# Optimization experiments

Hardware: AMD Instinct MI355X
Metric: run time of the kernel (lower is better)

## Reference

```python
import jax, jax.numpy as jnp
import numpy as np

DIM = 128
NUM_HEADS = 4
HEAD_DIM = DIM // NUM_HEADS
WINDOW = 7
N = WINDOW * WINDOW
B = 16384
SCALE = HEAD_DIM ** -0.5


def _relative_position_index(window_size: int) -> np.ndarray:
    coords_h = np.arange(window_size)
    coords_w = np.arange(window_size)
    coords = np.stack(np.meshgrid(coords_h, coords_w, indexing='ij'))  # [2, w, w]
    coords_flatten = coords.reshape(2, -1)  # [2, w*w]
    rel = coords_flatten[:, :, None] - coords_flatten[:, None, :]  # [2, N, N]
    rel = rel.transpose(1, 2, 0).copy()
    rel[:, :, 0] += window_size - 1
    rel[:, :, 1] += window_size - 1
    rel[:, :, 0] *= 2 * window_size - 1
    return rel.sum(-1).astype(np.int32)  # [N, N]


def setup_inputs() -> dict:
    key = jax.random.key(0)
    ks = jax.random.split(key, 8)
    x = jax.random.normal(ks[0], (B, N, DIM), dtype=jnp.float32)
    q_global = jax.random.normal(ks[1], (B, 1, DIM), dtype=jnp.float32)
    w_qkv = jax.random.normal(ks[2], (3 * DIM, DIM), dtype=jnp.float32) * (DIM ** -0.5)
    b_qkv = jnp.zeros((3 * DIM,), dtype=jnp.float32)
    w_proj = jax.random.normal(ks[3], (DIM, DIM), dtype=jnp.float32) * (DIM ** -0.5)
    b_proj = jnp.zeros((DIM,), dtype=jnp.float32)
    table_size = (2 * WINDOW - 1) * (2 * WINDOW - 1)
    bias_table = jax.random.normal(ks[4], (table_size, NUM_HEADS), dtype=jnp.float32) * 0.02
    rel_index = jnp.asarray(_relative_position_index(WINDOW))  # [N, N] int32
    return {"x": x, "q_global": q_global, "w_qkv": w_qkv, "b_qkv": b_qkv,
            "w_proj": w_proj, "b_proj": b_proj, "bias_table": bias_table,
            "rel_index": rel_index}


def reference(x, q_global, w_qkv, b_qkv, w_proj, b_proj, bias_table, rel_index):
    Bn, Nn, C = x.shape
    # qkv projection: [B, N, 3*C] -> [3, B, H, N, hd]
    qkv = (x @ w_qkv.T + b_qkv).reshape(Bn, Nn, 3, NUM_HEADS, HEAD_DIM)
    qkv = qkv.transpose(2, 0, 3, 1, 4)
    q, k, v = qkv[0], qkv[1], qkv[2]
    q = q * SCALE
    attn = jnp.einsum('bhnd,bhmd->bhnm', q, k)  # [B, H, N, N]
    # relative position bias: gather [N*N, H] -> [H, N, N]
    bias = bias_table[rel_index.reshape(-1)].reshape(Nn, Nn, NUM_HEADS).transpose(2, 0, 1)
    attn = attn + bias[None]
    attn = jax.nn.softmax(attn, axis=-1)
    out = jnp.einsum('bhnm,bhmd->bhnd', attn, v)  # [B, H, N, hd]
    out = out.transpose(0, 2, 1, 3).reshape(Bn, Nn, C)
    return out @ w_proj.T + b_proj
```

## Files before the change

kernel.cpp:

```cpp
#include <hip/hip_runtime.h>

#define NWIN 49
#define CDIM 128
#define SCALEQ 0.17677669529663687f
#define LOG2E  1.4426950408889634f

typedef _Float16 half8 __attribute__((ext_vector_type(8)));
typedef _Float16 half4v __attribute__((ext_vector_type(4)));
typedef float f32x4 __attribute__((ext_vector_type(4)));
typedef float f32x16 __attribute__((ext_vector_type(16)));

#define WS_WQKV  0
#define WS_WPROJ 49152
#define WS_BQKV  65536
#define WS_BIAS  65920
#define WS_TOTAL 78464

#define XL_STR 136
#define QK_STR 40
#define P_STR  72
#define VT_STR 72

#define XBUF_H  (64 * XL_STR)
#define K_OFF_H (64 * QK_STR)
#define HEAD_H  (2 * K_OFF_H)
#define VBUF_H  (32 * VT_STR)
#define SMEM_H  (XBUF_H + 4 * HEAD_H + 4 * VBUF_H)

__global__ __launch_bounds__(256)
void prepack(const float* __restrict__ w_qkv, const float* __restrict__ b_qkv,
             const float* __restrict__ w_proj, const float* __restrict__ bias_table,
             const int* __restrict__ rel_index, _Float16* __restrict__ ws)
{
    int i = blockIdx.x * 256 + threadIdx.x;
    if (i < 49152) {
        float v = w_qkv[i];
        if (i < 16384) v *= SCALEQ * LOG2E;
        ws[WS_WQKV + i] = (_Float16)v;
    } else if (i < 65536) {
        ws[i] = (_Float16)w_proj[i - 49152];
    } else if (i < 65920) {
        int n = i - 65536;
        float v = b_qkv[n];
        if (n < 128) v *= SCALEQ * LOG2E;
        ws[WS_BQKV + n] = (_Float16)v;
    } else if (i < WS_TOTAL) {
        int t = i - 65920;
        int h = t / 3136;
        int r = t - h * 3136;
        int q = r >> 6;
        int key = r & 63;
        float v = (key < 49) ? bias_table[(size_t)rel_index[q * 49 + key] * 4 + h] * LOG2E
                             : -1.44e4f;
        ws[WS_BIAS + t] = (_Float16)v;
    }
}

__global__ __launch_bounds__(512)
void lwa_fused(const float* __restrict__ x, const _Float16* __restrict__ ws,
               const float* __restrict__ b_proj, float* __restrict__ out,
               int nwin_total, int wpb)
{
    __shared__ __align__(16) _Float16 smem[SMEM_H];

    const int tid  = threadIdx.x;
    const int w    = tid >> 6;
    const int h    = w >> 1;
    const int c    = w & 1;
    const int lane = tid & 63;
    const int lo   = lane & 15;
    const int hi   = lane >> 4;
    const int ncol = 32 * h + 16 * c + lo;

    _Float16* const xb = smem;
    _Float16* const Qh = smem + XBUF_H + h * HEAD_H;
    _Float16* const Kh = Qh + K_OFF_H;
    _Float16* const Ph = Qh;
    _Float16* const Vh = smem + XBUF_H + 4 * HEAD_H + h * VBUF_H;

    const f32x4 zf = {0.f, 0.f, 0.f, 0.f};

    const int rt = w >> 2;
    const int ct = w & 3;
    const int cl = lane & 31;
    const int kh = lane >> 5;
    const float bpe3 = b_proj[32 * ct + cl];

    const int r0 = tid >> 4;
    const int gc = (tid & 15) * 8;

    int b0 = blockIdx.x * wpb;
    int b1 = b0 + wpb; if (b1 > nwin_total) b1 = nwin_total;

    {
        const float* xs = x + (size_t)b0 * NWIN * CDIM;
#pragma unroll
        for (int p = 0; p < 2; ++p) {
            int row = r0 + p * 32;
            if (row < 49) {
                const float* sp = xs + (size_t)row * CDIM + gc;
                float4 u0 = *reinterpret_cast<const float4*>(sp);
                float4 u1 = *reinterpret_cast<const float4*>(sp + 4);
                half8 hh;
                hh[0] = (_Float16)u0.x; hh[1] = (_Float16)u0.y;
                hh[2] = (_Float16)u0.z; hh[3] = (_Float16)u0.w;
                hh[4] = (_Float16)u1.x; hh[5] = (_Float16)u1.y;
                hh[6] = (_Float16)u1.z; hh[7] = (_Float16)u1.w;
                *reinterpret_cast<half8*>(&xb[row * XL_STR + gc]) = hh;
            }
        }
    }
    __syncthreads();

    for (int b = b0; b < b1; ++b) {
        const bool hn = (b + 1 < b1);

        float4 s0a, s0b, s1a, s1b;
        if (hn) {
            const float* xs = x + (size_t)(b + 1) * NWIN * CDIM;
            const float* sp0 = xs + (size_t)r0 * CDIM + gc;
            s0a = *reinterpret_cast<const float4*>(sp0);
            s0b = *reinterpret_cast<const float4*>(sp0 + 4);
            int row1 = r0 + 32;
            if (row1 < 49) {
                const float* sp1 = xs + (size_t)row1 * CDIM + gc;
                s1a = *reinterpret_cast<const float4*>(sp1);
                s1b = *reinterpret_cast<const float4*>(sp1 + 4);
            }
        }

        half8 wf0[4], wf1[4], wf2[4];
        {
            const _Float16* wp0 = ws + WS_WQKV + (size_t)ncol * CDIM + hi * 8;
            const _Float16* wp1 = wp0 + (size_t)CDIM * CDIM;
            const _Float16* wp2 = wp1 + (size_t)CDIM * CDIM;
#pragma unroll
            for (int kk = 0; kk < 4; ++kk) {
                wf0[kk] = *reinterpret_cast<const half8*>(wp0 + kk * 32);
                wf1[kk] = *reinterpret_cast<const half8*>(wp1 + kk * 32);
                wf2[kk] = *reinterpret_cast<const half8*>(wp2 + kk * 32);
            }
        }
        half4v bqq = *reinterpret_cast<const half4v*>(ws + WS_BQKV + 32 * h + 16 * c + 4 * hi);
        half4v bqk = *reinterpret_cast<const half4v*>(ws + WS_BQKV + CDIM + 32 * h + 16 * c + 4 * hi);
        float bq2 = (float)ws[WS_BQKV + 2 * CDIM + ncol];

#pragma unroll 1
        for (int tm = 0; tm < 4; ++tm) {
            int ar = 16 * tm + lo; if (ar > 48) ar = 48;
            const _Float16* ap = &xb[ar * XL_STR + hi * 8];
            half8 a0 = *reinterpret_cast<const half8*>(ap);
            half8 a1 = *reinterpret_cast<const half8*>(ap + 32);
            half8 a2 = *reinterpret_cast<const half8*>(ap + 64);
            half8 a3 = *reinterpret_cast<const half8*>(ap + 96);

            f32x4 aq; aq[0] = (float)bqq[0]; aq[1] = (float)bqq[1];
                      aq[2] = (float)bqq[2]; aq[3] = (float)bqq[3];
            aq = __builtin_amdgcn_mfma_f32_16x16x32_f16(wf0[0], a0, aq, 0, 0, 0);
            aq = __builtin_amdgcn_mfma_f32_16x16x32_f16(wf0[1], a1, aq, 0, 0, 0);
            aq = __builtin_amdgcn_mfma_f32_16x16x32_f16(wf0[2], a2, aq, 0, 0, 0);
            aq = __builtin_amdgcn_mfma_f32_16x16x32_f16(wf0[3], a3, aq, 0, 0, 0);

            f32x4 ak; ak[0] = (float)bqk[0]; ak[1] = (float)bqk[1];
                      ak[2] = (float)bqk[2]; ak[3] = (float)bqk[3];
            ak = __builtin_amdgcn_mfma_f32_16x16x32_f16(wf1[0], a0, ak, 0, 0, 0);
            ak = __builtin_amdgcn_mfma_f32_16x16x32_f16(wf1[1], a1, ak, 0, 0, 0);
            ak = __builtin_amdgcn_mfma_f32_16x16x32_f16(wf1[2], a2, ak, 0, 0, 0);
            ak = __builtin_amdgcn_mfma_f32_16x16x32_f16(wf1[3], a3, ak, 0, 0, 0);

            f32x4 av; av[0] = bq2; av[1] = bq2; av[2] = bq2; av[3] = bq2;
            av = __builtin_amdgcn_mfma_f32_16x16x32_f16(a0, wf2[0], av, 0, 0, 0);
            av = __builtin_amdgcn_mfma_f32_16x16x32_f16(a1, wf2[1], av, 0, 0, 0);
            av = __builtin_amdgcn_mfma_f32_16x16x32_f16(a2, wf2[2], av, 0, 0, 0);
            av = __builtin_amdgcn_mfma_f32_16x16x32_f16(a3, wf2[3], av, 0, 0, 0);

            half4v hq, hk;
#pragma unroll
            for (int j = 0; j < 4; ++j) { hq[j] = (_Float16)aq[j]; hk[j] = (_Float16)ak[j]; }
            *reinterpret_cast<half4v*>(&Qh[(16 * tm + lo) * QK_STR + 16 * c + 4 * hi]) = hq;
            *reinterpret_cast<half4v*>(&Kh[(16 * tm + lo) * QK_STR + 16 * c + 4 * hi]) = hk;

            half4v hv;
#pragma unroll
            for (int j = 0; j < 4; ++j) hv[j] = (_Float16)av[j];
            *reinterpret_cast<half4v*>(&Vh[(16 * c + lo) * VT_STR + 16 * tm + 4 * hi]) = hv;
        }
        __syncthreads();

        half8 kf[2], qf[4];
#pragma unroll
        for (int kt = 0; kt < 2; ++kt)
            kf[kt] = *reinterpret_cast<const half8*>(&Kh[(16 * (2 * c + kt) + lo) * QK_STR + hi * 8]);
#pragma unroll
        for (int t = 0; t < 4; ++t)
            qf[t] = *reinterpret_cast<const half8*>(&Qh[(16 * t + lo) * QK_STR + hi * 8]);
        __syncthreads();

#pragma unroll
        for (int tnq = 0; tnq < 4; ++tnq) {
            int q = 16 * tnq + lo;
            int qc = (q < 49) ? q : 48;
            const _Float16* bb = ws + WS_BIAS + ((size_t)h * 49 + qc) * 64 + 32 * c + 4 * hi;
            float sum = 0.f;
#pragma unroll
            for (int kt = 0; kt < 2; ++kt) {
                f32x4 s = __builtin_amdgcn_mfma_f32_16x16x32_f16(kf[kt], qf[tnq], zf, 0, 0, 0);
                half4v bt = *reinterpret_cast<const half4v*>(bb + kt * 16);
                half4v hv;
#pragma unroll
                for (int j = 0; j < 4; ++j) {
                    float pv = __builtin_amdgcn_exp2f(s[j] + (float)bt[j]);
                    sum += pv;
                    hv[j] = (_Float16)pv;
                }
                *reinterpret_cast<half4v*>(&Ph[q * P_STR + 32 * c + 16 * kt + 4 * hi]) = hv;
            }
            sum += __shfl_xor(sum, 16);
            sum += __shfl_xor(sum, 32);
            if (hi == 0)
                *reinterpret_cast<float*>(&Ph[q * P_STR + 64 + 2 * c]) = sum;
        }
        __syncthreads();

        {
            const _Float16* vp = &Vh[(16 * c + lo) * VT_STR + hi * 8];
            half8 vf0 = *reinterpret_cast<const half8*>(vp);
            half8 vf1 = *reinterpret_cast<const half8*>(vp + 32);
#pragma unroll
            for (int tnq = 0; tnq < 4; ++tnq) {
                int q = 16 * tnq + lo;
                half8 pf0 = *reinterpret_cast<const half8*>(&Ph[q * P_STR + hi * 8]);
                half8 pf1 = *reinterpret_cast<const half8*>(&Ph[q * P_STR + 32 + hi * 8]);
                f32x4 o = __builtin_amdgcn_mfma_f32_16x16x32_f16(vf0, pf0, zf, 0, 0, 0);
                o = __builtin_amdgcn_mfma_f32_16x16x32_f16(vf1, pf1, o, 0, 0, 0);
                float2 s2 = *reinterpret_cast<const float2*>(&Ph[q * P_STR + 64]);
                float invl = 1.0f / (s2.x + s2.y);
                half4v hv;
#pragma unroll
                for (int j = 0; j < 4; ++j) hv[j] = (_Float16)(o[j] * invl);
                *reinterpret_cast<half4v*>(&xb[q * XL_STR + 32 * h + 16 * c + 4 * hi]) = hv;
            }
        }
        __syncthreads();

        {
            const _Float16* wb3 = ws + WS_WPROJ + (size_t)(32 * ct + cl) * CDIM + kh * 8;
            half8 bfr[8];
#pragma unroll
            for (int kk = 0; kk < 8; ++kk)
                bfr[kk] = *reinterpret_cast<const half8*>(wb3 + kk * 16);

            f32x16 g;
#pragma unroll
            for (int r = 0; r < 16; ++r) g[r] = bpe3;

            const _Float16* oa = &xb[(32 * rt + cl) * XL_STR + kh * 8];
#pragma unroll
            for (int kk = 0; kk < 8; ++kk) {
                half8 af = *reinterpret_cast<const half8*>(oa + kk * 16);
                g = __builtin_amdgcn_mfma_f32_32x32x16_f16(af, bfr[kk], g, 0, 0, 0);
            }
#pragma unroll
            for (int r = 0; r < 16; ++r) {
                int row = 32 * rt + (r & 3) + 8 * (r >> 2) + 4 * kh;
                if (row < 49)
                    out[((size_t)b * NWIN + row) * CDIM + 32 * ct + cl] = g[r];
            }
        }
        __syncthreads();

        if (hn) {
            half8 hh;
            hh[0] = (_Float16)s0a.x; hh[1] = (_Float16)s0a.y;
            hh[2] = (_Float16)s0a.z; hh[3] = (_Float16)s0a.w;
            hh[4] = (_Float16)s0b.x; hh[5] = (_Float16)s0b.y;
            hh[6] = (_Float16)s0b.z; hh[7] = (_Float16)s0b.w;
            *reinterpret_cast<half8*>(&xb[r0 * XL_STR + gc]) = hh;
            int row1 = r0 + 32;
            if (row1 < 49) {
                half8 h2;
                h2[0] = (_Float16)s1a.x; h2[1] = (_Float16)s1a.y;
                h2[2] = (_Float16)s1a.z; h2[3] = (_Float16)s1a.w;
                h2[4] = (_Float16)s1b.x; h2[5] = (_Float16)s1b.y;
                h2[6] = (_Float16)s1b.z; h2[7] = (_Float16)s1b.w;
                *reinterpret_cast<half8*>(&xb[row1 * XL_STR + gc]) = h2;
            }
        }
        __syncthreads();
    }
}

extern "C" void kernel_launch(void* const* d_in, const int* in_sizes, int n_in,
                              void* d_out, int out_size, void* d_ws, size_t ws_size,
                              hipStream_t stream) {
    const float* x          = (const float*)d_in[0];
    const float* w_qkv      = (const float*)d_in[2];
    const float* b_qkv      = (const float*)d_in[3];
    const float* w_proj     = (const float*)d_in[4];
    const float* b_proj     = (const float*)d_in[5];
    const float* bias_table = (const float*)d_in[6];
    const int*   rel_index  = (const int*)d_in[7];

    _Float16* ws = (_Float16*)d_ws;

    prepack<<<(WS_TOTAL + 255) / 256, 256, 0, stream>>>(w_qkv, b_qkv, w_proj,
                                                        bias_table, rel_index, ws);

    const int nwin = in_sizes[0] / (NWIN * CDIM);
    const int wpb = 16;
    const int nblk = (nwin + wpb - 1) / wpb;

    lwa_fused<<<nblk, 512, 0, stream>>>(x, ws, b_proj, (float*)d_out,
                                        nwin, wpb);
}
```

Baseline: 318.9 us.

## Reuse V smem for attention output, drop a barrier, pack fp16 conversions

The attention output now goes to a separate buffer that reuses the V region, instead of going back into the x tile. V fragments are loaded into registers before the softmax barrier, which makes that reuse safe. This lets the next window's x tile be written to LDS right after the QKV projection, removing one __syncthreads per window. Element-wise float-to-half conversions are replaced with packed cvt_pkrtz, which cuts conversion instructions but rounds toward zero instead of to nearest.

Result: faster. 299.4 us (-6.1%).

```diff
diff --git a/kernel.cpp b/kernel.cpp
--- a/kernel.cpp
+++ b/kernel.cpp
@@ -21,11 +21,28 @@
 #define P_STR  72
 #define VT_STR 72
 
-#define XBUF_H  (64 * XL_STR)
+#define XBUF_H  (49 * XL_STR)
 #define K_OFF_H (64 * QK_STR)
 #define HEAD_H  (2 * K_OFF_H)
 #define VBUF_H  (32 * VT_STR)
-#define SMEM_H  (XBUF_H + 4 * HEAD_H + 4 * VBUF_H)
+#define VREG_H  (4 * VBUF_H)
+#define SMEM_H  (XBUF_H + 4 * HEAD_H + VREG_H)
+
+static __device__ __forceinline__ half4v pk4(float a, float b, float c, float d) {
+    auto p0 = __builtin_amdgcn_cvt_pkrtz(a, b);
+    auto p1 = __builtin_amdgcn_cvt_pkrtz(c, d);
+    int2 r = { __builtin_bit_cast(int, p0), __builtin_bit_cast(int, p1) };
+    return __builtin_bit_cast(half4v, r);
+}
+static __device__ __forceinline__ half8 pk8(float4 u0, float4 u1) {
+    auto p0 = __builtin_amdgcn_cvt_pkrtz(u0.x, u0.y);
+    auto p1 = __builtin_amdgcn_cvt_pkrtz(u0.z, u0.w);
+    auto p2 = __builtin_amdgcn_cvt_pkrtz(u1.x, u1.y);
+    auto p3 = __builtin_amdgcn_cvt_pkrtz(u1.z, u1.w);
+    int4 r = { __builtin_bit_cast(int, p0), __builtin_bit_cast(int, p1),
+               __builtin_bit_cast(int, p2), __builtin_bit_cast(int, p3) };
+    return __builtin_bit_cast(half8, r);
+}
 
 __global__ __launch_bounds__(256)
 void prepack(const float* __restrict__ w_qkv, const float* __restrict__ b_qkv,
@@ -77,6 +94,7 @@
     _Float16* const Kh = Qh + K_OFF_H;
     _Float16* const Ph = Qh;
     _Float16* const Vh = smem + XBUF_H + 4 * HEAD_H + h * VBUF_H;
+    _Float16* const Ob = smem + XBUF_H + 4 * HEAD_H;
 
     const f32x4 zf = {0.f, 0.f, 0.f, 0.f};
 
@@ -101,12 +119,7 @@
                 const float* sp = xs + (size_t)row * CDIM + gc;
                 float4 u0 = *reinterpret_cast<const float4*>(sp);
                 float4 u1 = *reinterpret_cast<const float4*>(sp + 4);
-                half8 hh;
-                hh[0] = (_Float16)u0.x; hh[1] = (_Float16)u0.y;
-                hh[2] = (_Float16)u0.z; hh[3] = (_Float16)u0.w;
-                hh[4] = (_Float16)u1.x; hh[5] = (_Float16)u1.y;
-                hh[6] = (_Float16)u1.z; hh[7] = (_Float16)u1.w;
-                *reinterpret_cast<half8*>(&xb[row * XL_STR + gc]) = hh;
+                *reinterpret_cast<half8*>(&xb[row * XL_STR + gc]) = pk8(u0, u1);
             }
         }
     }
@@ -174,26 +187,34 @@
             av = __builtin_amdgcn_mfma_f32_16x16x32_f16(a2, wf2[2], av, 0, 0, 0);
             av = __builtin_amdgcn_mfma_f32_16x16x32_f16(a3, wf2[3], av, 0, 0, 0);
 
-            half4v hq, hk;
-#pragma unroll
-            for (int j = 0; j < 4; ++j) { hq[j] = (_Float16)aq[j]; hk[j] = (_Float16)ak[j]; }
-            *reinterpret_cast<half4v*>(&Qh[(16 * tm + lo) * QK_STR + 16 * c + 4 * hi]) = hq;
-            *reinterpret_cast<half4v*>(&Kh[(16 * tm + lo) * QK_STR + 16 * c + 4 * hi]) = hk;
-
-            half4v hv;
-#pragma unroll
-            for (int j = 0; j < 4; ++j) hv[j] = (_Float16)av[j];
-            *reinterpret_cast<half4v*>(&Vh[(16 * c + lo) * VT_STR + 16 * tm + 4 * hi]) = hv;
-        }
-        __syncthreads();
-
-        half8 kf[2], qf[4];
+            *reinterpret_cast<half4v*>(&Qh[(16 * tm + lo) * QK_STR + 16 * c + 4 * hi]) =
+                pk4(aq[0], aq[1], aq[2], aq[3]);
+            *reinterpret_cast<half4v*>(&Kh[(16 * tm + lo) * QK_STR + 16 * c + 4 * hi]) =
+                pk4(ak[0], ak[1], ak[2], ak[3]);
+            *reinterpret_cast<half4v*>(&Vh[(16 * c + lo) * VT_STR + 16 * tm + 4 * hi]) =
+                pk4(av[0], av[1], av[2], av[3]);
+        }
+        __syncthreads();
+
+        if (hn) {
+            *reinterpret_cast<half8*>(&xb[r0 * XL_STR + gc]) = pk8(s0a, s0b);
+            int row1 = r0 + 32;
+            if (row1 < 49)
+                *reinterpret_cast<half8*>(&xb[row1 * XL_STR + gc]) = pk8(s1a, s1b);
+        }
+
+        half8 kf[2], qf[4], vf0, vf1;
 #pragma unroll
         for (int kt = 0; kt < 2; ++kt)
             kf[kt] = *reinterpret_cast<const half8*>(&Kh[(16 * (2 * c + kt) + lo) * QK_STR + hi * 8]);
 #pragma unroll
         for (int t = 0; t < 4; ++t)
             qf[t] = *reinterpret_cast<const half8*>(&Qh[(16 * t + lo) * QK_STR + hi * 8]);
+        {
+            const _Float16* vp = &Vh[(16 * c + lo) * VT_STR + hi * 8];
+            vf0 = *reinterpret_cast<const half8*>(vp);
+            vf1 = *reinterpret_cast<const half8*>(vp + 32);
+        }
         __syncthreads();
 
 #pragma unroll
@@ -206,14 +227,13 @@
             for (int kt = 0; kt < 2; ++kt) {
                 f32x4 s = __builtin_amdgcn_mfma_f32_16x16x32_f16(kf[kt], qf[tnq], zf, 0, 0, 0);
                 half4v bt = *reinterpret_cast<const half4v*>(bb + kt * 16);
-                half4v hv;
-#pragma unroll
-                for (int j = 0; j < 4; ++j) {
-                    float pv = __builtin_amdgcn_exp2f(s[j] + (float)bt[j]);
-                    sum += pv;
-                    hv[j] = (_Float16)pv;
-                }
-                *reinterpret_cast<half4v*>(&Ph[q * P_STR + 32 * c + 16 * kt + 4 * hi]) = hv;
+                float p0 = __builtin_amdgcn_exp2f(s[0] + (float)bt[0]);
+                float p1 = __builtin_amdgcn_exp2f(s[1] + (float)bt[1]);
+                float p2 = __builtin_amdgcn_exp2f(s[2] + (float)bt[2]);
+                float p3 = __builtin_amdgcn_exp2f(s[3] + (float)bt[3]);
+                sum += p0 + p1 + p2 + p3;
+                *reinterpret_cast<half4v*>(&Ph[q * P_STR + 32 * c + 16 * kt + 4 * hi]) =
+                    pk4(p0, p1, p2, p3);
             }
             sum += __shfl_xor(sum, 16);
             sum += __shfl_xor(sum, 32);
@@ -222,24 +242,17 @@
         }
         __syncthreads();
 
-        {
-            const _Float16* vp = &Vh[(16 * c + lo) * VT_STR + hi * 8];
-            half8 vf0 = *reinterpret_cast<const half8*>(vp);
-            half8 vf1 = *reinterpret_cast<const half8*>(vp + 32);
-#pragma unroll
-            for (int tnq = 0; tnq < 4; ++tnq) {
-                int q = 16 * tnq + lo;
-                half8 pf0 = *reinterpret_cast<const half8*>(&Ph[q * P_STR + hi * 8]);
-                half8 pf1 = *reinterpret_cast<const half8*>(&Ph[q * P_STR + 32 + hi * 8]);
-                f32x4 o = __builtin_amdgcn_mfma_f32_16x16x32_f16(vf0, pf0, zf, 0, 0, 0);
-                o = __builtin_amdgcn_mfma_f32_16x16x32_f16(vf1, pf1, o, 0, 0, 0);
-                float2 s2 = *reinterpret_cast<const float2*>(&Ph[q * P_STR + 64]);
-                float invl = 1.0f / (s2.x + s2.y);
-                half4v hv;
-#pragma unroll
-                for (int j = 0; j < 4; ++j) hv[j] = (_Float16)(o[j] * invl);
-                *reinterpret_cast<half4v*>(&xb[q * XL_STR + 32 * h + 16 * c + 4 * hi]) = hv;
-            }
+#pragma unroll
+        for (int tnq = 0; tnq < 4; ++tnq) {
+            int q = 16 * tnq + lo;
+            half8 pf0 = *reinterpret_cast<const half8*>(&Ph[q * P_STR + hi * 8]);
+            half8 pf1 = *reinterpret_cast<const half8*>(&Ph[q * P_STR + 32 + hi * 8]);
+            f32x4 o = __builtin_amdgcn_mfma_f32_16x16x32_f16(vf0, pf0, zf, 0, 0, 0);
+            o = __builtin_amdgcn_mfma_f32_16x16x32_f16(vf1, pf1, o, 0, 0, 0);
+            float2 s2 = *reinterpret_cast<const float2*>(&Ph[q * P_STR + 64]);
+            float invl = 1.0f / (s2.x + s2.y);
+            *reinterpret_cast<half4v*>(&Ob[q * XL_STR + 32 * h + 16 * c + 4 * hi]) =
+                pk4(o[0] * invl, o[1] * invl, o[2] * invl, o[3] * invl);
         }
         __syncthreads();
 
@@ -254,7 +267,7 @@
 #pragma unroll
             for (int r = 0; r < 16; ++r) g[r] = bpe3;
 
-            const _Float16* oa = &xb[(32 * rt + cl) * XL_STR + kh * 8];
+            const _Float16* oa = &Ob[(32 * rt + cl) * XL_STR + kh * 8];
 #pragma unroll
             for (int kk = 0; kk < 8; ++kk) {
                 half8 af = *reinterpret_cast<const half8*>(oa + kk * 16);
@@ -265,25 +278,6 @@
                 int row = 32 * rt + (r & 3) + 8 * (r >> 2) + 4 * kh;
                 if (row < 49)
                     out[((size_t)b * NWIN + row) * CDIM + 32 * ct + cl] = g[r];
-            }
-        }
-        __syncthreads();
-
-        if (hn) {
-            half8 hh;
-            hh[0] = (_Float16)s0a.x; hh[1] = (_Float16)s0a.y;
-            hh[2] = (_Float16)s0a.z; hh[3] = (_Float16)s0a.w;
-            hh[4] = (_Float16)s0b.x; hh[5] = (_Float16)s0b.y;
-            hh[6] = (_Float16)s0b.z; hh[7] = (_Float16)s0b.w;
-            *reinterpret_cast<half8*>(&xb[r0 * XL_STR + gc]) = hh;
-            int row1 = r0 + 32;
-            if (row1 < 49) {
-                half8 h2;
-                h2[0] = (_Float16)s1a.x; h2[1] = (_Float16)s1a.y;
-                h2[2] = (_Float16)s1a.z; h2[3] = (_Float16)s1a.w;
-                h2[4] = (_Float16)s1b.x; h2[5] = (_Float16)s1b.y;
-                h2[6] = (_Float16)s1b.z; h2[7] = (_Float16)s1b.w;
-                *reinterpret_cast<half8*>(&xb[row1 * XL_STR + gc]) = h2;
             }
         }
         __syncthreads();
```
